# Optimization experiments

Hardware: AMD Instinct MI355X
Metric: run time of the kernel (lower is better)

Reference implementation:

```python
import jax, jax.numpy as jnp
import numpy as np

VOCAB = 50000
EMB = 32
HID = 32
NUM_CLASSES = 2


def setup_inputs() -> dict:
    key = jax.random.key(0)
    ks = jax.random.split(key, 8)
    B, S = 1024, 512
    x = jax.random.randint(ks[0], (B, S), 0, VOCAB, dtype=jnp.int64)
    # embedding table has vocab_size + 1 rows, per `len(encoder.vocab) + 1`
    emb = jax.random.normal(ks[1], (VOCAB + 1, EMB), dtype=jnp.float32)
    s = 1.0 / np.sqrt(HID)
    w_ih = jax.random.uniform(ks[2], (4 * HID, EMB), jnp.float32, -s, s)
    w_hh = jax.random.uniform(ks[3], (4 * HID, HID), jnp.float32, -s, s)
    b_ih = jax.random.uniform(ks[4], (4 * HID,), jnp.float32, -s, s)
    b_hh = jax.random.uniform(ks[5], (4 * HID,), jnp.float32, -s, s)
    sf = 1.0 / np.sqrt(HID)
    fc_w = jax.random.uniform(ks[6], (NUM_CLASSES, HID), jnp.float32, -sf, sf)
    fc_b = jax.random.uniform(ks[7], (NUM_CLASSES,), jnp.float32, -sf, sf)
    return {"x": x, "emb": emb, "w_ih": w_ih, "w_hh": w_hh,
            "b_ih": b_ih, "b_hh": b_hh, "fc_w": fc_w, "fc_b": fc_b}


def _lstm_last_h(x, emb, w_ih, w_hh, b_ih, b_hh):
    xe = emb[x]                                        # [B, S, EMB]
    # precompute input-to-gate projection for all timesteps: [B, S, 4H]
    xp = jnp.einsum('bse,ge->bsg', xe, w_ih) + (b_ih + b_hh)
    B = x.shape[0]
    h0 = jnp.zeros((B, HID), xp.dtype)
    c0 = jnp.zeros((B, HID), xp.dtype)

    def step(carry, xt):
        h, c = carry
        gates = xt + h @ w_hh.T                        # [B, 4H]
        i, f, g, o = jnp.split(gates, 4, axis=-1)      # PyTorch gate order
        i = jax.nn.sigmoid(i)
        f = jax.nn.sigmoid(f)
        g = jnp.tanh(g)
        o = jax.nn.sigmoid(o)
        c = f * c + i * g
        h = o * jnp.tanh(c)
        return (h, c), None

    (h_n, c_n), _ = jax.lax.scan(step, (h0, c0), jnp.swapaxes(xp, 0, 1))
    return h_n                                          # last-timestep hidden


def reference(x, emb, w_ih, w_hh, b_ih, b_hh, fc_w, fc_b):
    h_last = _lstm_last_h(x, emb, w_ih, w_hh, b_ih, b_hh)
    return h_last @ fc_w.T + fc_b                       # [B, 2]
```

## Files before the change

kernel.cpp:

```cpp
#include <hip/hip_runtime.h>


#define LOG2E 1.44269504088896340736f

typedef float f32x32 __attribute__((ext_vector_type(32)));
typedef float f32x8 __attribute__((ext_vector_type(8)));

__device__ __forceinline__ float fast_rcp(float x) { return __builtin_amdgcn_rcpf(x); }
__device__ __forceinline__ float fast_exp2(float x) { return __builtin_amdgcn_exp2f(x); }

__device__ __forceinline__ float lane_bcast(float v, int srclane) {
    return __uint_as_float(__builtin_amdgcn_readlane(__float_as_uint(v), srclane));
}

__device__ __forceinline__ float bcast_hi(float x) {
#if __has_builtin(__builtin_amdgcn_permlane32_swap)
    typedef unsigned uv2 __attribute__((ext_vector_type(2)));
    uv2 r = __builtin_amdgcn_permlane32_swap(__float_as_uint(x), __float_as_uint(x),
                                             false, false);
    return __uint_as_float(r.y);
#else
    return __shfl_xor(x, 32, 64);
#endif
}

__global__ __launch_bounds__(64, 1) void build_ptab(
    const float4* __restrict__ emb4, const float4* __restrict__ wih4,
    const float* __restrict__ bih, const float* __restrict__ bhh,
    float2* __restrict__ ptab, int nrows) {
    const int lane = threadIdx.x;

    float w0[32], w1[32];
#pragma unroll
    for (int q = 0; q < 8; ++q) {
        float4 a = wih4[lane * 8 + q];
        float4 b = wih4[(lane + 64) * 8 + q];
        w0[4 * q + 0] = a.x; w0[4 * q + 1] = a.y; w0[4 * q + 2] = a.z; w0[4 * q + 3] = a.w;
        w1[4 * q + 0] = b.x; w1[4 * q + 1] = b.y; w1[4 * q + 2] = b.z; w1[4 * q + 3] = b.w;
    }
    const float bias0 = bih[lane] + bhh[lane];
    const float bias1 = bih[lane + 64] + bhh[lane + 64];
    const float s0 = -LOG2E;
    const float s1 = (lane < 32) ? (2.0f * LOG2E) : (-LOG2E);

    for (int v = blockIdx.x; v < nrows; v += gridDim.x) {
        float a0 = bias0, a1 = bias1;
#pragma unroll
        for (int q = 0; q < 8; ++q) {
            float4 e = emb4[v * 8 + q];
            a0 = fmaf(e.x, w0[4 * q + 0], a0);
            a0 = fmaf(e.y, w0[4 * q + 1], a0);
            a0 = fmaf(e.z, w0[4 * q + 2], a0);
            a0 = fmaf(e.w, w0[4 * q + 3], a0);
            a1 = fmaf(e.x, w1[4 * q + 0], a1);
            a1 = fmaf(e.y, w1[4 * q + 1], a1);
            a1 = fmaf(e.z, w1[4 * q + 2], a1);
            a1 = fmaf(e.w, w1[4 * q + 3], a1);
        }
        ptab[v * 64 + lane] = make_float2(a0 * s0, a1 * s1);
    }
}

#define STEP(G0, G1)                                                          \
    do {                                                                      \
        float _x0 = (G0), _x1 = 0.f, _x2 = 0.f, _x3 = 0.f;                    \
        float _y0 = (G1), _y1 = 0.f, _y2 = 0.f, _y3 = 0.f;                    \
        _Pragma("unroll") for (int _j = 0; _j < 32; _j += 4) {                \
            float _h0 = lane_bcast(h, _j + 0);                                \
            float _h1 = lane_bcast(h, _j + 1);                                \
            float _h2 = lane_bcast(h, _j + 2);                                \
            float _h3 = lane_bcast(h, _j + 3);                                \
            _x0 = fmaf(_h0, wf0[_j + 0], _x0);                                \
            _y0 = fmaf(_h0, wf1[_j + 0], _y0);                                \
            _x1 = fmaf(_h1, wf0[_j + 1], _x1);                                \
            _y1 = fmaf(_h1, wf1[_j + 1], _y1);                                \
            _x2 = fmaf(_h2, wf0[_j + 2], _x2);                                \
            _y2 = fmaf(_h2, wf1[_j + 2], _y2);                                \
            _x3 = fmaf(_h3, wf0[_j + 3], _x3);                                \
            _y3 = fmaf(_h3, wf1[_j + 3], _y3);                                \
        }                                                                     \
        float _a0 = (_x0 + _x1) + (_x2 + _x3);    \
        float _a1 = (_y0 + _y1) + (_y2 + _y3);    \
        float _sg = fast_rcp(1.0f + fast_exp2(_a0));        \
        float _r1 = fast_rcp(1.0f + fast_exp2(_a1));               \
        float _fg = bcast_hi(_sg);                                            \
        float _og = bcast_hi(_r1);                                            \
        float _gg = fmaf(-2.0f, _r1, 1.0f);                  \
        c = fmaf(_fg, c, _sg * _gg);                                          \
        float _e2 = fast_exp2(c * (2.0f * LOG2E));                            \
        h = _og * fmaf(-2.0f, fast_rcp(1.0f + _e2), 1.0f);                    \
    } while (0)

template <bool PTAB>
__global__ __launch_bounds__(64)
__attribute__((amdgpu_waves_per_eu(1, 1)))
void lstm_scan(
    const int* __restrict__ x,
    const float2* __restrict__ ptab,
    const float* __restrict__ emb,
    const float* __restrict__ wih,
    const float* __restrict__ bih,
    const float* __restrict__ bhh,
    const float* __restrict__ whh,
    const float* __restrict__ fcw,
    const float* __restrict__ fcb,
    float* __restrict__ out,
    int S) {
    extern __shared__ int xrow[];
    const int b = blockIdx.x;
    const int lane = threadIdx.x;

    for (int i = lane; i < S + 16; i += 64) xrow[i] = (i < S) ? x[(size_t)b * S + i] : 0;
    __syncthreads();

    const float s0 = -LOG2E;
    const float s1 = (lane < 32) ? (2.0f * LOG2E) : (-LOG2E);

    f32x32 wf0, wf1;
    {
        const float4* whh4 = (const float4*)whh;
#pragma unroll
        for (int q = 0; q < 8; ++q) {
            float4 a = whh4[lane * 8 + q];
            float4 bb = whh4[(lane + 64) * 8 + q];
            wf0[4 * q + 0] = a.x * s0; wf0[4 * q + 1] = a.y * s0;
            wf0[4 * q + 2] = a.z * s0; wf0[4 * q + 3] = a.w * s0;
            wf1[4 * q + 0] = bb.x * s1; wf1[4 * q + 1] = bb.y * s1;
            wf1[4 * q + 2] = bb.z * s1; wf1[4 * q + 3] = bb.w * s1;
        }
    }

    float h = 0.0f, c = 0.0f;

    if constexpr (PTAB) {
        int i0 = xrow[4], i1 = xrow[5], i2 = xrow[6], i3 = xrow[7];
        float2 p0 = ptab[(size_t)xrow[0] * 64 + lane];
        float2 p1 = ptab[(size_t)xrow[1] * 64 + lane];
        float2 p2 = ptab[(size_t)xrow[2] * 64 + lane];
        float2 p3 = ptab[(size_t)xrow[3] * 64 + lane];
        int t = 0;
        for (; t + 8 <= S; t += 4) {
            STEP(p0.x, p0.y); p0 = ptab[(size_t)i0 * 64 + lane]; i0 = xrow[t + 8];
            STEP(p1.x, p1.y); p1 = ptab[(size_t)i1 * 64 + lane]; i1 = xrow[t + 9];
            STEP(p2.x, p2.y); p2 = ptab[(size_t)i2 * 64 + lane]; i2 = xrow[t + 10];
            STEP(p3.x, p3.y); p3 = ptab[(size_t)i3 * 64 + lane]; i3 = xrow[t + 11];
        }
        if (t + 0 < S) STEP(p0.x, p0.y);
        if (t + 1 < S) STEP(p1.x, p1.y);
        if (t + 2 < S) STEP(p2.x, p2.y);
        if (t + 3 < S) STEP(p3.x, p3.y);
        if (t + 4 < S) { float2 q = ptab[(size_t)i0 * 64 + lane]; STEP(q.x, q.y); }
        if (t + 5 < S) { float2 q = ptab[(size_t)i1 * 64 + lane]; STEP(q.x, q.y); }
        if (t + 6 < S) { float2 q = ptab[(size_t)i2 * 64 + lane]; STEP(q.x, q.y); }
    } else {
        f32x32 wi0, wi1;
        {
            const float4* wih4 = (const float4*)wih;
#pragma unroll
            for (int q = 0; q < 8; ++q) {
                float4 a = wih4[lane * 8 + q];
                float4 bb = wih4[(lane + 64) * 8 + q];
                wi0[4 * q + 0] = a.x * s0; wi0[4 * q + 1] = a.y * s0;
                wi0[4 * q + 2] = a.z * s0; wi0[4 * q + 3] = a.w * s0;
                wi1[4 * q + 0] = bb.x * s1; wi1[4 * q + 1] = bb.y * s1;
                wi1[4 * q + 2] = bb.z * s1; wi1[4 * q + 3] = bb.w * s1;
            }
        }
        const float bias0 = (bih[lane] + bhh[lane]) * s0;
        const float bias1 = (bih[lane + 64] + bhh[lane + 64]) * s1;
        const float4* emb4 = (const float4*)emb;
        for (int t = 0; t < S; ++t) {
            int idx = xrow[t];
            float a0 = bias0, a1 = bias1;
#pragma unroll
            for (int q = 0; q < 8; ++q) {
                float4 e = emb4[(size_t)idx * 8 + q];
                a0 = fmaf(e.x, wi0[4 * q + 0], a0);
                a0 = fmaf(e.y, wi0[4 * q + 1], a0);
                a0 = fmaf(e.z, wi0[4 * q + 2], a0);
                a0 = fmaf(e.w, wi0[4 * q + 3], a0);
                a1 = fmaf(e.x, wi1[4 * q + 0], a1);
                a1 = fmaf(e.y, wi1[4 * q + 1], a1);
                a1 = fmaf(e.z, wi1[4 * q + 2], a1);
                a1 = fmaf(e.w, wi1[4 * q + 3], a1);
            }
            STEP(a0, a1);
        }
    }

    float wv0 = fcw[lane & 31];
    float wv1 = fcw[32 + (lane & 31)];
    float p0v = (lane < 32) ? h * wv0 : 0.0f;
    float p1v = (lane < 32) ? h * wv1 : 0.0f;
#pragma unroll
    for (int m = 32; m >= 1; m >>= 1) {
        p0v += __shfl_xor(p0v, m, 64);
        p1v += __shfl_xor(p1v, m, 64);
    }
    if (lane == 0) {
        out[b * 2 + 0] = p0v + fcb[0];
        out[b * 2 + 1] = p1v + fcb[1];
    }
}

extern "C" void kernel_launch(void* const* d_in, const int* in_sizes, int n_in,
                              void* d_out, int out_size, void* d_ws, size_t ws_size,
                              hipStream_t stream) {
    const int* x = (const int*)d_in[0];
    const float* emb = (const float*)d_in[1];
    const float* wih = (const float*)d_in[2];
    const float* whh = (const float*)d_in[3];
    const float* bih = (const float*)d_in[4];
    const float* bhh = (const float*)d_in[5];
    const float* fcw = (const float*)d_in[6];
    const float* fcb = (const float*)d_in[7];
    float* out = (float*)d_out;

    const int B = out_size / 2;
    const int S = in_sizes[0] / B;
    const int nrows = in_sizes[1] / 32;

    const size_t need = (size_t)nrows * 64 * sizeof(float2);
    const size_t smem = (size_t)(S + 16) * sizeof(int);

    if (ws_size >= need) {
        float2* ptab = (float2*)d_ws;
        int nb = nrows < 4096 ? nrows : 4096;
        build_ptab<<<nb, 64, 0, stream>>>((const float4*)emb, (const float4*)wih,
                                          bih, bhh, ptab, nrows);
        lstm_scan<true><<<B, 64, smem, stream>>>(x, ptab, emb, wih, bih, bhh, whh,
                                                 fcw, fcb, out, S);
    } else {
        lstm_scan<false><<<B, 64, smem, stream>>>(x, nullptr, emb, wih, bih, bhh, whh,
                                                  fcw, fcb, out, S);
    }
}
```

Measured before the change: 148.7 us.

## Replace readlane broadcasts with ds_swizzle XOR exchange and packed FMA recurrence

The per-step recurrent dot product no longer broadcasts each of the 32 hidden values with v_readlane. Each lane now pulls partner values with XOR-pattern ds_swizzle, and the W_hh weights are permuted per lane at load time to match that XOR order. The FMAs are issued as v_pk_fma_f32 on pairs, the gate exchange takes both halves from a single permlane32_swap, and the cell state is kept pre-scaled by 2*log2(e) to drop a multiply before the tanh exp2. The aim is to shorten the serial per-timestep chain; in exchange, swizzles go through the LDS crossbar and carry their own latency, and inline asm limits the compiler's scheduling.

```diff
diff --git a/kernel.cpp b/kernel.cpp
--- a/kernel.cpp
+++ b/kernel.cpp
@@ -3,26 +3,34 @@
 
 #define LOG2E 1.44269504088896340736f
 
+typedef float f32x2 __attribute__((ext_vector_type(2)));
+typedef unsigned uv2 __attribute__((ext_vector_type(2)));
 typedef float f32x32 __attribute__((ext_vector_type(32)));
-typedef float f32x8 __attribute__((ext_vector_type(8)));
 
 __device__ __forceinline__ float fast_rcp(float x) { return __builtin_amdgcn_rcpf(x); }
 __device__ __forceinline__ float fast_exp2(float x) { return __builtin_amdgcn_exp2f(x); }
 
-__device__ __forceinline__ float lane_bcast(float v, int srclane) {
-    return __uint_as_float(__builtin_amdgcn_readlane(__float_as_uint(v), srclane));
-}
-
-__device__ __forceinline__ float bcast_hi(float x) {
-#if __has_builtin(__builtin_amdgcn_permlane32_swap)
-    typedef unsigned uv2 __attribute__((ext_vector_type(2)));
+__device__ __forceinline__ f32x2 bcast_both(float x) {
     uv2 r = __builtin_amdgcn_permlane32_swap(__float_as_uint(x), __float_as_uint(x),
                                              false, false);
-    return __uint_as_float(r.y);
-#else
-    return __shfl_xor(x, 32, 64);
-#endif
-}
+    f32x2 o;
+    o.x = __uint_as_float(r.x);
+    o.y = __uint_as_float(r.y);
+    return o;
+}
+
+#define SWZ(V, K)                                                              \
+    __uint_as_float((unsigned)__builtin_amdgcn_ds_swizzle(                     \
+        (int)__float_as_uint(V), (((K) << 10) | 0x1F)))
+
+#define PKFMA(ACC, W, HK)                                                      \
+    {                                                                          \
+        f32x2 _d;                                                              \
+        asm("v_pk_fma_f32 %0, %1, %2, %3"                                      \
+            : "=v"(_d)                                                         \
+            : "v"(W), "v"(HK), "v"(ACC));                                      \
+        ACC = _d;                                                              \
+    }
 
 __global__ __launch_bounds__(64, 1) void build_ptab(
     const float4* __restrict__ emb4, const float4* __restrict__ wih4,
@@ -61,34 +69,61 @@
     }
 }
 
-#define STEP(G0, G1)                                                          \
-    do {                                                                      \
-        float _x0 = (G0), _x1 = 0.f, _x2 = 0.f, _x3 = 0.f;                    \
-        float _y0 = (G1), _y1 = 0.f, _y2 = 0.f, _y3 = 0.f;                    \
-        _Pragma("unroll") for (int _j = 0; _j < 32; _j += 4) {                \
-            float _h0 = lane_bcast(h, _j + 0);                                \
-            float _h1 = lane_bcast(h, _j + 1);                                \
-            float _h2 = lane_bcast(h, _j + 2);                                \
-            float _h3 = lane_bcast(h, _j + 3);                                \
-            _x0 = fmaf(_h0, wf0[_j + 0], _x0);                                \
-            _y0 = fmaf(_h0, wf1[_j + 0], _y0);                                \
-            _x1 = fmaf(_h1, wf0[_j + 1], _x1);                                \
-            _y1 = fmaf(_h1, wf1[_j + 1], _y1);                                \
-            _x2 = fmaf(_h2, wf0[_j + 2], _x2);                                \
-            _y2 = fmaf(_h2, wf1[_j + 2], _y2);                                \
-            _x3 = fmaf(_h3, wf0[_j + 3], _x3);                                \
-            _y3 = fmaf(_h3, wf1[_j + 3], _y3);                                \
-        }                                                                     \
-        float _a0 = (_x0 + _x1) + (_x2 + _x3);    \
-        float _a1 = (_y0 + _y1) + (_y2 + _y3);    \
-        float _sg = fast_rcp(1.0f + fast_exp2(_a0));        \
-        float _r1 = fast_rcp(1.0f + fast_exp2(_a1));               \
-        float _fg = bcast_hi(_sg);                                            \
-        float _og = bcast_hi(_r1);                                            \
-        float _gg = fmaf(-2.0f, _r1, 1.0f);                  \
-        c = fmaf(_fg, c, _sg * _gg);                                          \
-        float _e2 = fast_exp2(c * (2.0f * LOG2E));                            \
-        h = _og * fmaf(-2.0f, fast_rcp(1.0f + _e2), 1.0f);                    \
+#define REP16(M) M(0) M(1) M(2) M(3) M(4) M(5) M(6) M(7) M(8) M(9) M(10) M(11) \
+    M(12) M(13) M(14) M(15)
+
+#define WDECL(M) f32x2 w0_##M, w1_##M;
+#define WLOAD(M)                                                               \
+    {                                                                          \
+        int _c0 = (lane & 31) ^ (2 * (M));                                     \
+        int _c1 = _c0 ^ 1;                                                     \
+        w0_##M.x = whh[(size_t)lane * 32 + _c0] * s0;                          \
+        w0_##M.y = whh[(size_t)lane * 32 + _c1] * s0;                          \
+        w1_##M.x = whh[((size_t)lane + 64) * 32 + _c0] * s1;                   \
+        w1_##M.y = whh[((size_t)lane + 64) * 32 + _c1] * s1;                   \
+    }
+
+#define DOTP(M, ACC0, ACC1)                                                    \
+    {                                                                          \
+        f32x2 _hk;                                                             \
+        _hk.x = SWZ(h, 2 * (M));                                               \
+        _hk.y = SWZ(h, 2 * (M) + 1);                                           \
+        PKFMA(ACC0, w0_##M, _hk);                                              \
+        PKFMA(ACC1, w1_##M, _hk);                                              \
+    }
+
+#define STEP(P)                                                                \
+    do {                                                                       \
+        f32x2 _acc00, _acc01 = (f32x2)(0.0f);                                  \
+        f32x2 _acc10, _acc11 = (f32x2)(0.0f);                                  \
+        _acc00.x = (P).x; _acc00.y = 0.0f;                                     \
+        _acc10.x = (P).y; _acc10.y = 0.0f;                                     \
+        {                \
+            f32x2 _hk;                                                         \
+            _hk.x = h;                                                         \
+            _hk.y = SWZ(h, 1);                                                 \
+            PKFMA(_acc00, w0_0, _hk);                                          \
+            PKFMA(_acc10, w1_0, _hk);                                          \
+        }                                                                      \
+        DOTP(1, _acc01, _acc11) DOTP(2, _acc00, _acc10)                        \
+        DOTP(3, _acc01, _acc11) DOTP(4, _acc00, _acc10)                        \
+        DOTP(5, _acc01, _acc11) DOTP(6, _acc00, _acc10)                        \
+        DOTP(7, _acc01, _acc11) DOTP(8, _acc00, _acc10)                        \
+        DOTP(9, _acc01, _acc11) DOTP(10, _acc00, _acc10)                       \
+        DOTP(11, _acc01, _acc11) DOTP(12, _acc00, _acc10)                      \
+        DOTP(13, _acc01, _acc11) DOTP(14, _acc00, _acc10)                      \
+        DOTP(15, _acc01, _acc11)                                               \
+        f32x2 _s0 = _acc00 + _acc01;                                           \
+        f32x2 _s1 = _acc10 + _acc11;                                           \
+        float _A0 = _s0.x + _s0.y;                 \
+        float _A1 = _s1.x + _s1.y;                 \
+        float _sg = fast_rcp(1.0f + fast_exp2(_A0));           \
+        float _r1 = fast_rcp(1.0f + fast_exp2(_A1));           \
+        f32x2 _bs = bcast_both(_sg);                \
+        f32x2 _br = bcast_both(_r1);               \
+        float _ggs = fmaf(-4.0f * LOG2E, _br.x, 2.0f * LOG2E);  \
+        cs = fmaf(_bs.y, cs, _bs.x * _ggs);                                    \
+        h = _br.y * fmaf(-2.0f, fast_rcp(1.0f + fast_exp2(cs)), 1.0f);         \
     } while (0)
 
 template <bool PTAB>
@@ -116,42 +151,32 @@
     const float s0 = -LOG2E;
     const float s1 = (lane < 32) ? (2.0f * LOG2E) : (-LOG2E);
 
-    f32x32 wf0, wf1;
-    {
-        const float4* whh4 = (const float4*)whh;
-#pragma unroll
-        for (int q = 0; q < 8; ++q) {
-            float4 a = whh4[lane * 8 + q];
-            float4 bb = whh4[(lane + 64) * 8 + q];
-            wf0[4 * q + 0] = a.x * s0; wf0[4 * q + 1] = a.y * s0;
-            wf0[4 * q + 2] = a.z * s0; wf0[4 * q + 3] = a.w * s0;
-            wf1[4 * q + 0] = bb.x * s1; wf1[4 * q + 1] = bb.y * s1;
-            wf1[4 * q + 2] = bb.z * s1; wf1[4 * q + 3] = bb.w * s1;
-        }
-    }
-
-    float h = 0.0f, c = 0.0f;
+    REP16(WDECL)
+    REP16(WLOAD)
+
+    float h = 0.0f, cs = 0.0f;
 
     if constexpr (PTAB) {
+        const char* pb = (const char*)ptab + (unsigned)(lane << 3);
         int i0 = xrow[4], i1 = xrow[5], i2 = xrow[6], i3 = xrow[7];
-        float2 p0 = ptab[(size_t)xrow[0] * 64 + lane];
-        float2 p1 = ptab[(size_t)xrow[1] * 64 + lane];
-        float2 p2 = ptab[(size_t)xrow[2] * 64 + lane];
-        float2 p3 = ptab[(size_t)xrow[3] * 64 + lane];
+        f32x2 p0 = *(const f32x2*)(pb + ((unsigned)xrow[0] << 9));
+        f32x2 p1 = *(const f32x2*)(pb + ((unsigned)xrow[1] << 9));
+        f32x2 p2 = *(const f32x2*)(pb + ((unsigned)xrow[2] << 9));
+        f32x2 p3 = *(const f32x2*)(pb + ((unsigned)xrow[3] << 9));
         int t = 0;
         for (; t + 8 <= S; t += 4) {
-            STEP(p0.x, p0.y); p0 = ptab[(size_t)i0 * 64 + lane]; i0 = xrow[t + 8];
-            STEP(p1.x, p1.y); p1 = ptab[(size_t)i1 * 64 + lane]; i1 = xrow[t + 9];
-            STEP(p2.x, p2.y); p2 = ptab[(size_t)i2 * 64 + lane]; i2 = xrow[t + 10];
-            STEP(p3.x, p3.y); p3 = ptab[(size_t)i3 * 64 + lane]; i3 = xrow[t + 11];
-        }
-        if (t + 0 < S) STEP(p0.x, p0.y);
-        if (t + 1 < S) STEP(p1.x, p1.y);
-        if (t + 2 < S) STEP(p2.x, p2.y);
-        if (t + 3 < S) STEP(p3.x, p3.y);
-        if (t + 4 < S) { float2 q = ptab[(size_t)i0 * 64 + lane]; STEP(q.x, q.y); }
-        if (t + 5 < S) { float2 q = ptab[(size_t)i1 * 64 + lane]; STEP(q.x, q.y); }
-        if (t + 6 < S) { float2 q = ptab[(size_t)i2 * 64 + lane]; STEP(q.x, q.y); }
+            STEP(p0); p0 = *(const f32x2*)(pb + ((unsigned)i0 << 9)); i0 = xrow[t + 8];
+            STEP(p1); p1 = *(const f32x2*)(pb + ((unsigned)i1 << 9)); i1 = xrow[t + 9];
+            STEP(p2); p2 = *(const f32x2*)(pb + ((unsigned)i2 << 9)); i2 = xrow[t + 10];
+            STEP(p3); p3 = *(const f32x2*)(pb + ((unsigned)i3 << 9)); i3 = xrow[t + 11];
+        }
+        if (t + 0 < S) STEP(p0);
+        if (t + 1 < S) STEP(p1);
+        if (t + 2 < S) STEP(p2);
+        if (t + 3 < S) STEP(p3);
+        if (t + 4 < S) { f32x2 q = *(const f32x2*)(pb + ((unsigned)i0 << 9)); STEP(q); }
+        if (t + 5 < S) { f32x2 q = *(const f32x2*)(pb + ((unsigned)i1 << 9)); STEP(q); }
+        if (t + 6 < S) { f32x2 q = *(const f32x2*)(pb + ((unsigned)i2 << 9)); STEP(q); }
     } else {
         f32x32 wi0, wi1;
         {
@@ -184,7 +209,8 @@
                 a1 = fmaf(e.z, wi1[4 * q + 2], a1);
                 a1 = fmaf(e.w, wi1[4 * q + 3], a1);
             }
-            STEP(a0, a1);
+            f32x2 _p; _p.x = a0; _p.y = a1;
+            STEP(_p);
         }
     }
 
```

Result: slower. 265.2 us (+78.3%).
